# Kernel optimization log

Hardware: AMD Instinct MI355X
Metric: run time of the kernel (lower is better)

The kernel has to match this reference:

```python
import jax, jax.numpy as jnp
import numpy as np

N_NODES = 100000
N_EDGES = 1600000
FEAT = 32
HID = 32
N_GRAPHS = 64


def setup_inputs() -> dict:
    key = jax.random.key(0)
    ks = jax.random.split(key, 12)
    x = jax.random.normal(ks[0], (N_NODES, FEAT), dtype=jnp.float32)
    edge_index = jax.random.randint(ks[1], (2, N_EDGES), 0, N_NODES, dtype=jnp.int64)
    batch = jnp.sort(jax.random.randint(ks[2], (N_NODES,), 0, N_GRAPHS, dtype=jnp.int64))
    # ChebConv (K=3) params: one linear per Chebyshev order + shared bias
    W_cheb = jax.random.normal(ks[3], (3, FEAT, HID), dtype=jnp.float32) * 0.1
    b_cheb = jnp.zeros((HID,), dtype=jnp.float32)
    # MLP head 32 -> 1024 -> 512 -> 4
    W1 = jax.random.normal(ks[4], (HID, 1024), dtype=jnp.float32) * 0.05
    b1 = jnp.zeros((1024,), dtype=jnp.float32)
    W2 = jax.random.normal(ks[5], (1024, 512), dtype=jnp.float32) * 0.05
    b2 = jnp.zeros((512,), dtype=jnp.float32)
    W3 = jax.random.normal(ks[6], (512, 4), dtype=jnp.float32) * 0.05
    b3 = jnp.zeros((4,), dtype=jnp.float32)
    return {"x": x, "edge_index": edge_index, "batch": batch,
            "W_cheb": W_cheb, "b_cheb": b_cheb,
            "W1": W1, "b1": b1, "W2": W2, "b2": b2, "W3": W3, "b3": b3}


def reference(x, edge_index, batch, W_cheb, b_cheb, W1, b1, W2, b2, W3, b3):
    row, col = edge_index[0], edge_index[1]  # source, target
    n = x.shape[0]
    # symmetric normalization of scaled Laplacian (lambda_max=2, no self loops):
    # L_hat = -D^{-1/2} A D^{-1/2}
    deg = jax.ops.segment_sum(jnp.ones((row.shape[0],), x.dtype), row, num_segments=n)
    dis = jnp.where(deg > 0, jax.lax.rsqrt(jnp.where(deg > 0, deg, 1.0)), 0.0)
    norm = -(dis[row] * dis[col])  # [E]

    def prop(h):  # L_hat @ h via gather -> scale -> scatter-add
        return jax.ops.segment_sum(norm[:, None] * h[row], col, num_segments=n)

    # Chebyshev recursion: T0=x, T1=L_hat x, T2=2 L_hat T1 - T0
    Tx0 = x
    Tx1 = prop(Tx0)
    Tx2 = 2.0 * prop(Tx1) - Tx0
    h = Tx0 @ W_cheb[0] + Tx1 @ W_cheb[1] + Tx2 @ W_cheb[2] + b_cheb  # [N, HID]
    # global max pool per graph
    g = jax.ops.segment_max(h, batch, num_segments=N_GRAPHS)  # [B, HID]
    # MLP head (dropout/LeakyReLU defined but unused in original forward)
    h1 = jax.nn.relu(g @ W1 + b1)
    h2 = jax.nn.relu(h1 @ W2 + b2)
    return h2 @ W3 + b3  # [B, 4]
```

## Files before the change

### kernel.cpp

```cpp
#include <hip/hip_runtime.h>
#include <hip/hip_fp16.h>


#define NT 256
#define BSHIFT 8
#define BSIZE 256
#define HB 256
#define CAP 5120

typedef _Float16 half8 __attribute__((ext_vector_type(8)));
typedef float f32x4 __attribute__((ext_vector_type(4)));

__device__ __forceinline__ void atomicMaxFloat(float* addr, float val) {
    if (val >= 0.0f) atomicMax((int*)addr, __float_as_int(val));
    else             atomicMin((unsigned int*)addr, __float_as_uint(val));
}

#define ACC8(raw)                                        \
    do {                                                 \
        const __half2* hp_ = (const __half2*)&(raw);     \
        float2 f0_ = __half22float2(hp_[0]);             \
        float2 f1_ = __half22float2(hp_[1]);             \
        float2 f2_ = __half22float2(hp_[2]);             \
        float2 f3_ = __half22float2(hp_[3]);             \
        a0 += f0_.x; a1 += f0_.y; a2 += f1_.x; a3 += f1_.y; \
        a4 += f2_.x; a5 += f2_.y; a6 += f3_.x; a7 += f3_.y; \
    } while (0)

__global__ __launch_bounds__(512) void k_init(float* __restrict__ g,
                                              const float* __restrict__ Wc,
                                              _Float16* __restrict__ wfrag,
                                              int* __restrict__ bcur,
                                              int* __restrict__ rcur, int NBK) {
    int tid = threadIdx.x;
    for (int i = tid; i < 64 * 32; i += 512) g[i] = -__builtin_inff();
    if (tid < 384) {
        int combo = tid >> 6, lane = tid & 63;
        int mat = combo >> 1, n = combo & 1;
        int m = lane & 15, quad = lane >> 4;
        #pragma unroll
        for (int j = 0; j < 8; j++)
            wfrag[(size_t)combo * 512 + lane * 8 + j] =
                (_Float16)Wc[mat * 1024 + (quad * 8 + j) * 32 + n * 16 + m];
    }
    if (tid < NBK) {
        bcur[tid] = tid * CAP;
        rcur[tid] = tid * CAP;
    }
}

__global__ __launch_bounds__(NT) void k_bscatter3(const int* __restrict__ row,
                                                  const int* __restrict__ col,
                                                  int* __restrict__ bcur, int* __restrict__ rcur,
                                                  int* __restrict__ ebuck,
                                                  unsigned char* __restrict__ rbuck,
                                                  int E, int NBK, int epb) {
    __shared__ int lhc[512], lhr[512], lbasec[512], lbaser[512];
    int tid = threadIdx.x;
    for (int i = tid; i < NBK; i += NT) { lhc[i] = 0; lhr[i] = 0; }
    __syncthreads();
    int start = blockIdx.x * epb;
    int end = min(start + epb, E);
    for (int e = start + tid; e < end; e += NT) {
        atomicAdd(&lhc[col[e] >> BSHIFT], 1);
        atomicAdd(&lhr[row[e] >> BSHIFT], 1);
    }
    __syncthreads();
    for (int i = tid; i < NBK; i += NT) {
        int vc = lhc[i], vr = lhr[i];
        lbasec[i] = vc ? atomicAdd(&bcur[i], vc) : 0;
        lbaser[i] = vr ? atomicAdd(&rcur[i], vr) : 0;
        lhc[i] = 0;
        lhr[i] = 0;
    }
    __syncthreads();
    for (int e = start + tid; e < end; e += NT) {
        int r = row[e], c = col[e];
        int bc_ = c >> BSHIFT;
        int li = atomicAdd(&lhc[bc_], 1);
        ebuck[lbasec[bc_] + li] = (r << BSHIFT) | (c & (BSIZE - 1));
        int br_ = r >> BSHIFT;
        int lj = atomicAdd(&lhr[br_], 1);
        rbuck[lbaser[br_] + lj] = (unsigned char)(r & (BSIZE - 1));
    }
}

__global__ __launch_bounds__(NT) void k_prep(
    const int* __restrict__ rcur, const unsigned char* __restrict__ rbuck,
    const int* __restrict__ bcur, const int* __restrict__ ebuck,
    const float* __restrict__ x,
    float* __restrict__ dis, float* __restrict__ rdis,
    __half* __restrict__ xh, __half* __restrict__ xsh,
    int* __restrict__ offs, int* __restrict__ entries, int N) {
    __shared__ int cnt[1024];
    __shared__ int tsum[256];
    __shared__ float sdis[256];
    int b = blockIdx.x, tid = threadIdx.x;
    int rbase = b * CAP, rend = rcur[b];
    int ebase = b * CAP, eend = bcur[b];
    cnt[tid] = 0; cnt[tid + 256] = 0; cnt[tid + 512] = 0; cnt[tid + 768] = 0;
    __syncthreads();
    for (int e = rbase + tid; e < rend; e += NT)
        atomicAdd(&cnt[rbuck[e]], 1);
    __syncthreads();
    int dcount = cnt[tid];
    int node = (b << BSHIFT) + tid;
    float d = (dcount > 0) ? rsqrtf((float)dcount) : 0.0f;
    if (node < N) {
        dis[node] = d;
        rdis[node] = (dcount > 0) ? sqrtf((float)dcount) : 0.0f;
    }
    sdis[tid] = d;
    __syncthreads();
    cnt[tid] = 0; cnt[tid + 256] = 0; cnt[tid + 512] = 0; cnt[tid + 768] = 0;
    __syncthreads();
    for (int e = ebase + tid; e < eend; e += NT) {
        int pv = ebuck[e];
        atomicAdd(&cnt[((pv & (BSIZE - 1)) << 2) | ((pv >> BSHIFT) >> 15)], 1);
    }
    __syncthreads();
    int s0 = cnt[tid * 4], s1 = cnt[tid * 4 + 1], s2 = cnt[tid * 4 + 2], s3 = cnt[tid * 4 + 3];
    int tot = s0 + s1 + s2 + s3;
    tsum[tid] = tot;
    __syncthreads();
    for (int off = 1; off < 256; off <<= 1) {
        int t = (tid >= off) ? tsum[tid - off] : 0;
        __syncthreads();
        tsum[tid] += t;
        __syncthreads();
    }
    int excl = tsum[tid] - tot;
    if (node < N) offs[node] = ((ebase + excl) << 9) | tot;
    cnt[tid * 4]     = ebase + excl;
    cnt[tid * 4 + 1] = ebase + excl + s0;
    cnt[tid * 4 + 2] = ebase + excl + s0 + s1;
    cnt[tid * 4 + 3] = ebase + excl + s0 + s1 + s2;
    __syncthreads();
    for (int e = ebase + tid; e < eend; e += NT) {
        int pv = ebuck[e];
        int src = pv >> BSHIFT;
        int li = atomicAdd(&cnt[((pv & (BSIZE - 1)) << 2) | (src >> 15)], 1);
        entries[li] = src;
    }
    int nodebase = b << BSHIFT;
    for (int i4 = tid; i4 < 2048; i4 += NT) {
        int gnode = nodebase + (i4 >> 3);
        if (gnode >= N) break;
        float4 v = ((const float4*)x)[(size_t)nodebase * 8 + i4];
        float dd = sdis[i4 >> 3];
        float2 o, os;
        ((__half2*)&o)[0] = __floats2half2_rn(v.x, v.y);
        ((__half2*)&o)[1] = __floats2half2_rn(v.z, v.w);
        ((__half2*)&os)[0] = __floats2half2_rn(dd * v.x, dd * v.y);
        ((__half2*)&os)[1] = __floats2half2_rn(dd * v.z, dd * v.w);
        ((float2*)xh)[(size_t)nodebase * 8 + i4] = o;
        ((float2*)xsh)[(size_t)nodebase * 8 + i4] = os;
    }
}

__global__ __launch_bounds__(NT) void k_prop1(const int* __restrict__ offs,
                                              const int* __restrict__ entries,
                                              const float* __restrict__ dis,
                                              const __half* __restrict__ xsh,
                                              __half* __restrict__ xs2h, int N) {
    int idx = blockIdx.x * blockDim.x + threadIdx.x;
    int node = idx >> 3, sp = (idx >> 2) & 1, q = idx & 3;
    if (node >= N) return;
    int pv = offs[node];
    int s = pv >> 9, deg = pv & 511;
    int mid = s + (deg >> 1), t = s + deg;
    int lo = sp ? mid : s;
    int hi = sp ? t : mid;
    float a0 = 0, a1 = 0, a2 = 0, a3 = 0, a4 = 0, a5 = 0, a6 = 0, a7 = 0;
    for (int e = lo; e < hi; e++) {
        int r = entries[e];
        float4 w = *(const float4*)(xsh + (size_t)r * 32 + q * 8);
        ACC8(w);
    }
    a0 += __shfl_xor(a0, 4); a1 += __shfl_xor(a1, 4);
    a2 += __shfl_xor(a2, 4); a3 += __shfl_xor(a3, 4);
    a4 += __shfl_xor(a4, 4); a5 += __shfl_xor(a5, 4);
    a6 += __shfl_xor(a6, 4); a7 += __shfl_xor(a7, 4);
    if (sp == 0) {
        float d = dis[node];
        float sd = -d * d;
        float4 ov;
        ((__half2*)&ov)[0] = __floats2half2_rn(sd * a0, sd * a1);
        ((__half2*)&ov)[1] = __floats2half2_rn(sd * a2, sd * a3);
        ((__half2*)&ov)[2] = __floats2half2_rn(sd * a4, sd * a5);
        ((__half2*)&ov)[3] = __floats2half2_rn(sd * a6, sd * a7);
        *(float4*)(xs2h + (size_t)node * 32 + q * 8) = ov;
    }
}

__global__ __launch_bounds__(NT) void k_combine_f(
    const int* __restrict__ offs, const int* __restrict__ entries,
    const float* __restrict__ dis, const float* __restrict__ rdis,
    const __half* __restrict__ xs2h, const _Float16* __restrict__ xh,
    const _Float16* __restrict__ wfrag, const float* __restrict__ bc,
    const int* __restrict__ batch, float* __restrict__ g, int N) {
    __shared__ float sb[32];
    __shared__ float sp2[64][33];
    __shared__ float hs[64][33];
    __shared__ int sbatch[64];

    int tid = threadIdx.x;
    if (tid < 32) sb[tid] = bc[tid];
    int rowbase = blockIdx.x * 64;
    if (tid >= 64 && tid < 128) {
        int gr = rowbase + tid - 64;
        sbatch[tid - 64] = (gr < N) ? batch[gr] : -1;
    }

    int node_l = tid >> 2, q = tid & 3;
    int gnode = rowbase + node_l;
    if (gnode < N) {
        int pv = offs[gnode];
        int s = pv >> 9, t = s + (pv & 511);
        float a0 = 0, a1 = 0, a2 = 0, a3 = 0, a4 = 0, a5 = 0, a6 = 0, a7 = 0;
        for (int e = s; e < t; e++) {
            int r = entries[e];
            float4 w = *(const float4*)(xs2h + (size_t)r * 32 + q * 8);
            ACC8(w);
        }
        float sc = -dis[gnode];
        float* p = &sp2[node_l][q * 8];
        p[0] = sc * a0; p[1] = sc * a1; p[2] = sc * a2; p[3] = sc * a3;
        p[4] = sc * a4; p[5] = sc * a5; p[6] = sc * a6; p[7] = sc * a7;
    }
    __syncthreads();

    int wave = tid >> 6;
    int lane = tid & 63;
    int m = lane & 15;
    int quad = lane >> 4;
    int grow = rowbase + wave * 16 + m;

    half8 a0 = {}, a1 = {}, a2 = {};
    if (grow < N) {
        size_t off = (size_t)grow * 32 + quad * 8;
        a0 = *(const half8*)(xh + off);
        half8 x2 = *(const half8*)((const _Float16*)xs2h + off);
        float rd = rdis[grow];
        const float* p = &sp2[wave * 16 + m][quad * 8];
        #pragma unroll
        for (int j = 0; j < 8; j++) {
            a1[j] = (_Float16)((float)x2[j] * rd);
            a2[j] = (_Float16)(2.0f * p[j] - (float)a0[j]);
        }
    }

    const half8* wf = (const half8*)wfrag;
    f32x4 acc[2];
    #pragma unroll
    for (int n = 0; n < 2; n++) {
        f32x4 c = {0.f, 0.f, 0.f, 0.f};
        c = __builtin_amdgcn_mfma_f32_16x16x32_f16(a0, wf[(0 * 2 + n) * 64 + lane], c, 0, 0, 0);
        c = __builtin_amdgcn_mfma_f32_16x16x32_f16(a1, wf[(1 * 2 + n) * 64 + lane], c, 0, 0, 0);
        c = __builtin_amdgcn_mfma_f32_16x16x32_f16(a2, wf[(2 * 2 + n) * 64 + lane], c, 0, 0, 0);
        acc[n] = c;
    }

    #pragma unroll
    for (int n = 0; n < 2; n++)
        #pragma unroll
        for (int r = 0; r < 4; r++)
            hs[wave * 16 + quad * 4 + r][n * 16 + m] = acc[n][r] + sb[n * 16 + m];
    __syncthreads();

    int f = tid & 31, s = tid >> 5;
    int curb = -1;
    float curm = 0.0f;
    for (int j = s * 8; j < s * 8 + 8; j++) {
        int b = sbatch[j];
        if (b < 0) continue;
        float v = hs[j][f];
        if (b != curb) {
            if (curb >= 0) atomicMaxFloat(&g[curb * 32 + f], curm);
            curb = b;
            curm = v;
        } else {
            curm = fmaxf(curm, v);
        }
    }
    if (curb >= 0) atomicMaxFloat(&g[curb * 32 + f], curm);
}

__global__ __launch_bounds__(NT) void k_mlp12(const float* __restrict__ g,
                                              const float* __restrict__ W1,
                                              const float* __restrict__ b1,
                                              const float* __restrict__ W2,
                                              float* __restrict__ h2acc) {
    __shared__ float sg[32];
    __shared__ float sh[128];
    int gi = blockIdx.x >> 3, ks = blockIdx.x & 7;
    int tid = threadIdx.x;
    if (tid < 32) sg[tid] = g[gi * 32 + tid];
    __syncthreads();
    if (tid < 128) {
        int c = ks * 128 + tid;
        float a = b1[c];
        #pragma unroll
        for (int k = 0; k < 32; k++) a += sg[k] * W1[k * 1024 + c];
        sh[tid] = fmaxf(a, 0.0f);
    }
    __syncthreads();
    const float* w = W2 + (size_t)(ks * 128) * 512;
    float acc0 = 0.0f, acc1 = 0.0f;
    for (int k = 0; k < 128; k++) {
        float h = sh[k];
        acc0 += h * w[k * 512 + tid];
        acc1 += h * w[k * 512 + tid + 256];
    }
    atomicAdd(&h2acc[gi * 512 + tid], acc0);
    atomicAdd(&h2acc[gi * 512 + tid + 256], acc1);
}

__global__ __launch_bounds__(NT) void k_mlp3p(const float* __restrict__ h2acc,
                                              const float* __restrict__ b2,
                                              const float* __restrict__ W3,
                                              const float* __restrict__ b3,
                                              float* __restrict__ out) {
    __shared__ float sp[256];
    int gi = blockIdx.x;
    int tid = threadIdx.x;
    int j = tid & 3, slot = tid >> 2;
    float part = 0.0f;
    #pragma unroll
    for (int kk = 0; kk < 8; kk++) {
        int k = slot * 8 + kk;
        float h = fmaxf(h2acc[gi * 512 + k] + b2[k], 0.0f);
        part += h * W3[k * 4 + j];
    }
    sp[tid] = part;
    __syncthreads();
    for (int s = 32; s >= 1; s >>= 1) {
        if (slot < s) sp[tid] += sp[(slot + s) * 4 + j];
        __syncthreads();
    }
    if (slot == 0) out[gi * 4 + j] = sp[j] + b3[j];
}

extern "C" void kernel_launch(void* const* d_in, const int* in_sizes, int n_in,
                              void* d_out, int out_size, void* d_ws, size_t ws_size,
                              hipStream_t stream) {
    const float* x   = (const float*)d_in[0];
    const int* ei    = (const int*)d_in[1];
    const int* batch = (const int*)d_in[2];
    const float* Wc  = (const float*)d_in[3];
    const float* bc  = (const float*)d_in[4];
    const float* W1  = (const float*)d_in[5];
    const float* b1  = (const float*)d_in[6];
    const float* W2  = (const float*)d_in[7];
    const float* b2  = (const float*)d_in[8];
    const float* W3  = (const float*)d_in[9];
    const float* b3  = (const float*)d_in[10];
    float* out       = (float*)d_out;

    const int N = in_sizes[2];
    const int E = in_sizes[1] / 2;
    const int* row = ei;
    const int* col = ei + E;
    const int NBK = (N + BSIZE - 1) / BSIZE;
    const int epb = (E + HB - 1) / HB;
    const size_t PADE = (size_t)NBK * CAP;

    float* h2acc    = (float*)d_ws;
    int* bcur       = (int*)(h2acc + 64 * 512);
    int* rcur       = bcur + 512;
    float* dis      = (float*)(rcur + 512);
    float* rdis     = dis + N;
    int* offs       = (int*)(rdis + N);
    int* ebuck      = offs + N + 4;
    unsigned char* rbuck = (unsigned char*)(ebuck + PADE);
    int* entries    = (int*)(rbuck + PADE);
    _Float16* xh    = (_Float16*)(entries + PADE);
    _Float16* xsh   = xh + (size_t)N * 32;
    _Float16* xs2h  = xsh + (size_t)N * 32;
    float* g        = (float*)(xs2h + (size_t)N * 32);
    _Float16* wfrag = (_Float16*)(g + 64 * 32);

    hipMemsetAsync(h2acc, 0, sizeof(float) * 64 * 512, stream);

    k_init<<<1, 512, 0, stream>>>(g, Wc, wfrag, bcur, rcur, NBK);
    k_bscatter3<<<HB, NT, 0, stream>>>(row, col, bcur, rcur, ebuck, rbuck, E, NBK, epb);
    k_prep<<<NBK, NT, 0, stream>>>(rcur, rbuck, bcur, ebuck, x, dis, rdis,
                                   (__half*)xh, (__half*)xsh, offs, entries, N);
    k_prop1<<<((size_t)N * 8 + NT - 1) / NT, NT, 0, stream>>>(offs, entries, dis, (const __half*)xsh, (__half*)xs2h, N);
    k_combine_f<<<(N + 63) / 64, NT, 0, stream>>>(offs, entries, dis, rdis, (const __half*)xs2h, xh, wfrag, bc, batch, g, N);
    k_mlp12<<<512, NT, 0, stream>>>(g, W1, b1, W2, h2acc);
    k_mlp3p<<<64, NT, 0, stream>>>(h2acc, b2, W3, b3, out);
}
```

Baseline: 225.0 us.

## Replace row-bucket degree histogram with direct global atomic degree counts

```diff
diff --git a/kernel.cpp b/kernel.cpp
--- a/kernel.cpp
+++ b/kernel.cpp
@@ -3,9 +3,10 @@
 
 
 #define NT 256
+#define NTS 1024
 #define BSHIFT 8
 #define BSIZE 256
-#define HB 256
+#define HB 512
 #define CAP 5120
 
 typedef _Float16 half8 __attribute__((ext_vector_type(8)));
@@ -30,8 +31,7 @@
 __global__ __launch_bounds__(512) void k_init(float* __restrict__ g,
                                               const float* __restrict__ Wc,
                                               _Float16* __restrict__ wfrag,
-                                              int* __restrict__ bcur,
-                                              int* __restrict__ rcur, int NBK) {
+                                              int* __restrict__ bcur, int NBK) {
     int tid = threadIdx.x;
     for (int i = tid; i < 64 * 32; i += 512) g[i] = -__builtin_inff();
     if (tid < 384) {
@@ -43,50 +43,41 @@
             wfrag[(size_t)combo * 512 + lane * 8 + j] =
                 (_Float16)Wc[mat * 1024 + (quad * 8 + j) * 32 + n * 16 + m];
     }
-    if (tid < NBK) {
-        bcur[tid] = tid * CAP;
-        rcur[tid] = tid * CAP;
-    }
-}
-
-__global__ __launch_bounds__(NT) void k_bscatter3(const int* __restrict__ row,
+    if (tid < NBK) bcur[tid] = tid * CAP;
+}
+
+__global__ __launch_bounds__(NTS) void k_bscatter(const int* __restrict__ row,
                                                   const int* __restrict__ col,
-                                                  int* __restrict__ bcur, int* __restrict__ rcur,
+                                                  int* __restrict__ bcur,
+                                                  int* __restrict__ degcnt,
                                                   int* __restrict__ ebuck,
-                                                  unsigned char* __restrict__ rbuck,
                                                   int E, int NBK, int epb) {
-    __shared__ int lhc[512], lhr[512], lbasec[512], lbaser[512];
-    int tid = threadIdx.x;
-    for (int i = tid; i < NBK; i += NT) { lhc[i] = 0; lhr[i] = 0; }
+    __shared__ int lhc[512], lbasec[512];
+    int tid = threadIdx.x;
+    for (int i = tid; i < NBK; i += NTS) lhc[i] = 0;
     __syncthreads();
     int start = blockIdx.x * epb;
     int end = min(start + epb, E);
-    for (int e = start + tid; e < end; e += NT) {
+    for (int e = start + tid; e < end; e += NTS)
         atomicAdd(&lhc[col[e] >> BSHIFT], 1);
-        atomicAdd(&lhr[row[e] >> BSHIFT], 1);
-    }
-    __syncthreads();
-    for (int i = tid; i < NBK; i += NT) {
-        int vc = lhc[i], vr = lhr[i];
+    __syncthreads();
+    for (int i = tid; i < NBK; i += NTS) {
+        int vc = lhc[i];
         lbasec[i] = vc ? atomicAdd(&bcur[i], vc) : 0;
-        lbaser[i] = vr ? atomicAdd(&rcur[i], vr) : 0;
         lhc[i] = 0;
-        lhr[i] = 0;
-    }
-    __syncthreads();
-    for (int e = start + tid; e < end; e += NT) {
+    }
+    __syncthreads();
+    for (int e = start + tid; e < end; e += NTS) {
         int r = row[e], c = col[e];
+        atomicAdd(&degcnt[r], 1);
         int bc_ = c >> BSHIFT;
         int li = atomicAdd(&lhc[bc_], 1);
         ebuck[lbasec[bc_] + li] = (r << BSHIFT) | (c & (BSIZE - 1));
-        int br_ = r >> BSHIFT;
-        int lj = atomicAdd(&lhr[br_], 1);
-        rbuck[lbaser[br_] + lj] = (unsigned char)(r & (BSIZE - 1));
     }
 }
 
 __global__ __launch_bounds__(NT) void k_prep(
-    const int* __restrict__ rcur, const unsigned char* __restrict__ rbuck,
+    const int* __restrict__ degcnt,
     const int* __restrict__ bcur, const int* __restrict__ ebuck,
     const float* __restrict__ x,
     float* __restrict__ dis, float* __restrict__ rdis,
@@ -96,23 +87,16 @@
     __shared__ int tsum[256];
     __shared__ float sdis[256];
     int b = blockIdx.x, tid = threadIdx.x;
-    int rbase = b * CAP, rend = rcur[b];
     int ebase = b * CAP, eend = bcur[b];
     cnt[tid] = 0; cnt[tid + 256] = 0; cnt[tid + 512] = 0; cnt[tid + 768] = 0;
-    __syncthreads();
-    for (int e = rbase + tid; e < rend; e += NT)
-        atomicAdd(&cnt[rbuck[e]], 1);
-    __syncthreads();
-    int dcount = cnt[tid];
     int node = (b << BSHIFT) + tid;
+    int dcount = (node < N) ? degcnt[node] : 0;
     float d = (dcount > 0) ? rsqrtf((float)dcount) : 0.0f;
     if (node < N) {
         dis[node] = d;
         rdis[node] = (dcount > 0) ? sqrtf((float)dcount) : 0.0f;
     }
     sdis[tid] = d;
-    __syncthreads();
-    cnt[tid] = 0; cnt[tid + 256] = 0; cnt[tid + 512] = 0; cnt[tid + 768] = 0;
     __syncthreads();
     for (int e = ebase + tid; e < eend; e += NT) {
         int pv = ebuck[e];
@@ -366,25 +350,24 @@
     const size_t PADE = (size_t)NBK * CAP;
 
     float* h2acc    = (float*)d_ws;
-    int* bcur       = (int*)(h2acc + 64 * 512);
-    int* rcur       = bcur + 512;
-    float* dis      = (float*)(rcur + 512);
+    int* degcnt     = (int*)(h2acc + 64 * 512);
+    int* bcur       = degcnt + N;
+    float* dis      = (float*)(bcur + 512);
     float* rdis     = dis + N;
     int* offs       = (int*)(rdis + N);
     int* ebuck      = offs + N + 4;
-    unsigned char* rbuck = (unsigned char*)(ebuck + PADE);
-    int* entries    = (int*)(rbuck + PADE);
+    int* entries    = ebuck + PADE;
     _Float16* xh    = (_Float16*)(entries + PADE);
     _Float16* xsh   = xh + (size_t)N * 32;
     _Float16* xs2h  = xsh + (size_t)N * 32;
     float* g        = (float*)(xs2h + (size_t)N * 32);
     _Float16* wfrag = (_Float16*)(g + 64 * 32);
 
-    hipMemsetAsync(h2acc, 0, sizeof(float) * 64 * 512, stream);
-
-    k_init<<<1, 512, 0, stream>>>(g, Wc, wfrag, bcur, rcur, NBK);
-    k_bscatter3<<<HB, NT, 0, stream>>>(row, col, bcur, rcur, ebuck, rbuck, E, NBK, epb);
-    k_prep<<<NBK, NT, 0, stream>>>(rcur, rbuck, bcur, ebuck, x, dis, rdis,
+    hipMemsetAsync(h2acc, 0, sizeof(float) * 64 * 512 + sizeof(int) * N, stream);
+
+    k_init<<<1, 512, 0, stream>>>(g, Wc, wfrag, bcur, NBK);
+    k_bscatter<<<HB, NTS, 0, stream>>>(row, col, bcur, degcnt, ebuck, E, NBK, epb);
+    k_prep<<<NBK, NT, 0, stream>>>(degcnt, bcur, ebuck, x, dis, rdis,
                                    (__half*)xh, (__half*)xsh, offs, entries, N);
     k_prop1<<<((size_t)N * 8 + NT - 1) / NT, NT, 0, stream>>>(offs, entries, dis, (const __half*)xsh, (__half*)xs2h, N);
     k_combine_f<<<(N + 63) / 64, NT, 0, stream>>>(offs, entries, dis, rdis, (const __half*)xs2h, xh, wfrag, bc, batch, g, N);
```

Result: slower. 265.6 us (+18.0%).

## Stage edge bucket scatter in LDS with single pass and coalesced flush

Applied to the files above, without the earlier changes.

```diff
diff --git a/kernel.cpp b/kernel.cpp
--- a/kernel.cpp
+++ b/kernel.cpp
@@ -3,9 +3,12 @@
 
 
 #define NT 256
+#define NTS 1024
 #define BSHIFT 8
 #define BSIZE 256
 #define HB 256
+#define CAPC 48
+#define CAPR 64
 #define CAP 5120
 
 typedef _Float16 half8 __attribute__((ext_vector_type(8)));
@@ -49,39 +52,55 @@
     }
 }
 
-__global__ __launch_bounds__(NT) void k_bscatter3(const int* __restrict__ row,
+__global__ __launch_bounds__(NTS) void k_bscatter(const int* __restrict__ row,
                                                   const int* __restrict__ col,
-                                                  int* __restrict__ bcur, int* __restrict__ rcur,
+                                                  int* __restrict__ bcur,
+                                                  int* __restrict__ rcur,
                                                   int* __restrict__ ebuck,
                                                   unsigned char* __restrict__ rbuck,
                                                   int E, int NBK, int epb) {
-    __shared__ int lhc[512], lhr[512], lbasec[512], lbaser[512];
+    __shared__ int cntc[512], cntr[512];
+    __shared__ int basec[512], baser[512];
+    __shared__ int cstage[512 * CAPC];
+    __shared__ unsigned char rstage[512 * CAPR];
     int tid = threadIdx.x;
-    for (int i = tid; i < NBK; i += NT) { lhc[i] = 0; lhr[i] = 0; }
+    if (tid < 512) { cntc[tid] = 0; cntr[tid] = 0; }
     __syncthreads();
     int start = blockIdx.x * epb;
     int end = min(start + epb, E);
-    for (int e = start + tid; e < end; e += NT) {
-        atomicAdd(&lhc[col[e] >> BSHIFT], 1);
-        atomicAdd(&lhr[row[e] >> BSHIFT], 1);
-    }
-    __syncthreads();
-    for (int i = tid; i < NBK; i += NT) {
-        int vc = lhc[i], vr = lhr[i];
-        lbasec[i] = vc ? atomicAdd(&bcur[i], vc) : 0;
-        lbaser[i] = vr ? atomicAdd(&rcur[i], vr) : 0;
-        lhc[i] = 0;
-        lhr[i] = 0;
-    }
-    __syncthreads();
-    for (int e = start + tid; e < end; e += NT) {
+    for (int e = start + tid; e < end; e += NTS) {
         int r = row[e], c = col[e];
         int bc_ = c >> BSHIFT;
-        int li = atomicAdd(&lhc[bc_], 1);
-        ebuck[lbasec[bc_] + li] = (r << BSHIFT) | (c & (BSIZE - 1));
+        int li = atomicAdd(&cntc[bc_], 1);
+        if (li < CAPC)
+            cstage[bc_ * CAPC + li] = (r << BSHIFT) | (c & (BSIZE - 1));
         int br_ = r >> BSHIFT;
-        int lj = atomicAdd(&lhr[br_], 1);
-        rbuck[lbaser[br_] + lj] = (unsigned char)(r & (BSIZE - 1));
+        int lj = atomicAdd(&cntr[br_], 1);
+        if (lj < CAPR)
+            rstage[br_ * CAPR + lj] = (unsigned char)(r & (BSIZE - 1));
+    }
+    __syncthreads();
+    if (tid < 512) {
+        int n = min(cntc[tid], CAPC);
+        basec[tid] = n ? atomicAdd(&bcur[tid], n) : 0;
+    } else {
+        int b = tid - 512;
+        int n = min(cntr[b], CAPR);
+        baser[b] = n ? atomicAdd(&rcur[b], n) : 0;
+    }
+    __syncthreads();
+    int warp = tid >> 6, lane = tid & 63;
+    for (int b = warp; b < NBK; b += (NTS >> 6)) {
+        int n = min(cntc[b], CAPC);
+        int base = basec[b];
+        for (int i = lane; i < n; i += 64)
+            ebuck[base + i] = cstage[b * CAPC + i];
+    }
+    for (int b = warp; b < NBK; b += (NTS >> 6)) {
+        int n = min(cntr[b], CAPR);
+        int base = baser[b];
+        for (int i = lane; i < n; i += 64)
+            rbuck[base + i] = rstage[b * CAPR + i];
     }
 }
 
@@ -383,7 +402,7 @@
     hipMemsetAsync(h2acc, 0, sizeof(float) * 64 * 512, stream);
 
     k_init<<<1, 512, 0, stream>>>(g, Wc, wfrag, bcur, rcur, NBK);
-    k_bscatter3<<<HB, NT, 0, stream>>>(row, col, bcur, rcur, ebuck, rbuck, E, NBK, epb);
+    k_bscatter<<<HB, NTS, 0, stream>>>(row, col, bcur, rcur, ebuck, rbuck, E, NBK, epb);
     k_prep<<<NBK, NT, 0, stream>>>(rcur, rbuck, bcur, ebuck, x, dis, rdis,
                                    (__half*)xh, (__half*)xsh, offs, entries, N);
     k_prop1<<<((size_t)N * 8 + NT - 1) / NT, NT, 0, stream>>>(offs, entries, dis, (const __half*)xsh, (__half*)xs2h, N);
```

Result: faster. 210.3 us (-6.5%).
